# Kernel optimization log

Hardware: AMD Instinct MI355X
Metric: run time of the kernel (lower is better)

The kernel has to match this reference:

```python
import jax, jax.numpy as jnp
import numpy as np

N_NODES = 100000
N_EDGES = 1600000
IN_C = 256
H1 = 128
H2 = 64
OUT_C = 64


def setup_inputs() -> dict:
    key = jax.random.key(0)
    ks = jax.random.split(key, 8)
    x = jax.random.normal(ks[0], (N_NODES, IN_C), dtype=jnp.float32)
    edge_src = jax.random.randint(ks[1], (N_EDGES,), 0, N_NODES, dtype=jnp.int32)
    edge_dst = jax.random.randint(ks[2], (N_EDGES,), 0, N_NODES, dtype=jnp.int32)
    edge_weight = jax.random.uniform(ks[3], (N_EDGES,), dtype=jnp.float32)
    W1 = jax.random.normal(ks[4], (IN_C, H1), dtype=jnp.float32) / np.sqrt(IN_C)
    b1 = jnp.zeros((H1,), dtype=jnp.float32)
    W2 = jax.random.normal(ks[5], (H1, H2), dtype=jnp.float32) / np.sqrt(H1)
    b2 = jnp.zeros((H2,), dtype=jnp.float32)
    W3 = jax.random.normal(ks[6], (H2, OUT_C), dtype=jnp.float32) / np.sqrt(H2)
    b3 = jnp.zeros((OUT_C,), dtype=jnp.float32)
    return dict(x=x, edge_src=edge_src, edge_dst=edge_dst, edge_weight=edge_weight,
                W1=W1, b1=b1, W2=W2, b2=b2, W3=W3, b3=b3)


def _gcn_layer(h, W, b, src, dst, ew):
    # GraphConvolution: out = adj @ (h @ W) + b, adj given as weighted edge list
    support = h @ W                      # [N, d_out] dense GEMM
    msg = support[src] * ew[:, None]     # [E, d_out] gather (irregular access)
    agg = jax.ops.segment_sum(msg, dst, num_segments=N_NODES)  # SpMM scatter-add
    return agg + b


def reference(x, edge_src, edge_dst, edge_weight, W1, b1, W2, b2, W3, b3):
    # Eval-mode forward: dropout is identity (training=False)
    h = jax.nn.relu(_gcn_layer(x, W1, b1, edge_src, edge_dst, edge_weight))
    h = jax.nn.relu(_gcn_layer(h, W2, b2, edge_src, edge_dst, edge_weight))
    out = _gcn_layer(h, W3, b3, edge_src, edge_dst, edge_weight)
    return out
```

## Files before the change

### kernel.cpp

```cpp
#include <hip/hip_runtime.h>
#include <hip/hip_bf16.h>


#define EPB 8192

__device__ __forceinline__ unsigned short f2bf(float f) {
    unsigned int u = __float_as_uint(f);
    unsigned int r = (u + 0x7fffu + ((u >> 16) & 1u)) >> 16;
    return (unsigned short)r;
}

using frag_ab = __attribute__((ext_vector_type(8))) short;
using frag_cd = __attribute__((ext_vector_type(4))) float;

template <int BN, bool ABF16>
__global__ __launch_bounds__(256) void mfma_gemm_kernel(
    const void* __restrict__ Av, const unsigned short* __restrict__ WT,
    unsigned short* __restrict__ C, int M, int K)
{
    constexpr int BM = 128, BK = 64;
    constexpr int LDA = BK + 8;
    __shared__ unsigned short As[BM * LDA];
    __shared__ unsigned short Bs[BN * LDA];

    const int tid = threadIdx.x;
    const int wave = tid >> 6;
    const int lane = tid & 63;
    const int quad = lane >> 4;
    const int l16 = lane & 15;
    const int m0 = blockIdx.x * BM;

    frag_cd acc[2][BN / 16];
#pragma unroll
    for (int rt = 0; rt < 2; ++rt)
#pragma unroll
        for (int f = 0; f < BN / 16; ++f) acc[rt][f] = (frag_cd){0.f, 0.f, 0.f, 0.f};

    for (int k0 = 0; k0 < K; k0 += BK) {
        if constexpr (!ABF16) {
            const float* A = (const float*)Av;
#pragma unroll
            for (int i = 0; i < 8; ++i) {
                const int linear = (i * 256 + tid) * 4;
                const int r = linear >> 6;
                const int c = linear & 63;
                const int row = m0 + r;
                float4 v = make_float4(0.f, 0.f, 0.f, 0.f);
                if (row < M) v = *(const float4*)&A[(size_t)row * K + k0 + c];
                ushort4 u;
                u.x = f2bf(v.x); u.y = f2bf(v.y); u.z = f2bf(v.z); u.w = f2bf(v.w);
                *(ushort4*)&As[r * LDA + c] = u;
            }
        } else {
            const unsigned short* A = (const unsigned short*)Av;
#pragma unroll
            for (int i = 0; i < 4; ++i) {
                const int linear = (i * 256 + tid) * 8;
                const int r = linear >> 6;
                const int c = linear & 63;
                const int row = m0 + r;
                uint4 u = make_uint4(0u, 0u, 0u, 0u);
                if (row < M) u = *(const uint4*)&A[(size_t)row * K + k0 + c];
                *(uint4*)&As[r * LDA + c] = u;
            }
        }
#pragma unroll
        for (int i = 0; i < BN / 32; ++i) {
            const int linear = (i * 256 + tid) * 8;
            const int n = linear >> 6;
            const int c = linear & 63;
            const uint4 u = *(const uint4*)&WT[(size_t)n * K + k0 + c];
            *(uint4*)&Bs[n * LDA + c] = u;
        }
        __syncthreads();

#pragma unroll
        for (int ks = 0; ks < 2; ++ks) {
            const int kk = ks * 32 + quad * 8;
            const frag_ab a0 = *(const frag_ab*)&As[(wave * 32 + l16) * LDA + kk];
            const frag_ab a1 = *(const frag_ab*)&As[(wave * 32 + 16 + l16) * LDA + kk];
#pragma unroll
            for (int f = 0; f < BN / 16; ++f) {
                const frag_ab b = *(const frag_ab*)&Bs[(f * 16 + l16) * LDA + kk];
                acc[0][f] = __builtin_amdgcn_mfma_f32_16x16x32_bf16(a0, b, acc[0][f], 0, 0, 0);
                acc[1][f] = __builtin_amdgcn_mfma_f32_16x16x32_bf16(a1, b, acc[1][f], 0, 0, 0);
            }
        }
        __syncthreads();
    }

#pragma unroll
    for (int rt = 0; rt < 2; ++rt)
#pragma unroll
        for (int f = 0; f < BN / 16; ++f)
#pragma unroll
            for (int r = 0; r < 4; ++r) {
                const int row = m0 + wave * 32 + rt * 16 + quad * 4 + r;
                if (row < M) C[(size_t)row * BN + f * 16 + l16] = f2bf(acc[rt][f][r]);
            }
}

__global__ __launch_bounds__(256) void wt_kernel(
    const float* __restrict__ W1, const float* __restrict__ W2, const float* __restrict__ W3,
    unsigned short* __restrict__ WT1, unsigned short* __restrict__ WT2, unsigned short* __restrict__ WT3)
{
    const int i = blockIdx.x * 256 + threadIdx.x;
    const float* W; unsigned short* WT; int K, N, j;
    if (i < 32768)      { W = W1; WT = WT1; K = 256; N = 128; j = i; }
    else if (i < 40960) { W = W2; WT = WT2; K = 128; N = 64;  j = i - 32768; }
    else if (i < 45056) { W = W3; WT = WT3; K = 64;  N = 64;  j = i - 40960; }
    else return;
    const int n = j / K, k = j % K;
    WT[j] = f2bf(W[k * N + n]);
}

__global__ __launch_bounds__(256) void count_kernel(
    const int* __restrict__ dst, int* __restrict__ cmat, int E, int nblk, int nbuck)
{
    __shared__ int hist[1600];
    for (int i = threadIdx.x; i < nbuck; i += 256) hist[i] = 0;
    __syncthreads();
    const int base = blockIdx.x * EPB;
    const int end = min(base + EPB, E);
    for (int e = base + threadIdx.x; e < end; e += 256)
        atomicAdd(&hist[dst[e] >> 6], 1);
    __syncthreads();
    for (int i = threadIdx.x; i < nbuck; i += 256)
        cmat[(size_t)i * nblk + blockIdx.x] = hist[i];
}

__global__ __launch_bounds__(256) void scanA_kernel(
    int* __restrict__ data, int* __restrict__ psum, int L)
{
    __shared__ int tmp[256];
    const int b0 = blockIdx.x * 1024 + threadIdx.x * 4;
    int v[4] = {0, 0, 0, 0};
    if (b0 + 3 < L) { const int4 t = *(const int4*)&data[b0]; v[0]=t.x; v[1]=t.y; v[2]=t.z; v[3]=t.w; }
    else { for (int i = 0; i < 4; ++i) if (b0 + i < L) v[i] = data[b0 + i]; }
    const int s = v[0] + v[1] + v[2] + v[3];
    tmp[threadIdx.x] = s;
    __syncthreads();
#pragma unroll
    for (int d = 1; d < 256; d <<= 1) {
        const int t = (threadIdx.x >= d) ? tmp[threadIdx.x - d] : 0;
        __syncthreads();
        tmp[threadIdx.x] += t;
        __syncthreads();
    }
    int run = tmp[threadIdx.x] - s;
    int o[4];
#pragma unroll
    for (int i = 0; i < 4; ++i) { o[i] = run; run += v[i]; }
    if (b0 + 3 < L) { *(int4*)&data[b0] = make_int4(o[0], o[1], o[2], o[3]); }
    else { for (int i = 0; i < 4; ++i) if (b0 + i < L) data[b0 + i] = o[i]; }
    if (threadIdx.x == 255) psum[blockIdx.x] = tmp[255];
}

__global__ __launch_bounds__(1024) void scanB_kernel(int* __restrict__ psum, int nb)
{
    __shared__ int tmp[1024];
    const int v = ((int)threadIdx.x < nb) ? psum[threadIdx.x] : 0;
    tmp[threadIdx.x] = v;
    __syncthreads();
#pragma unroll
    for (int d = 1; d < 1024; d <<= 1) {
        const int t = ((int)threadIdx.x >= d) ? tmp[threadIdx.x - d] : 0;
        __syncthreads();
        tmp[threadIdx.x] += t;
        __syncthreads();
    }
    if ((int)threadIdx.x < nb) psum[threadIdx.x] = tmp[threadIdx.x] - v;
}

__global__ __launch_bounds__(256) void scanC_kernel(
    int* __restrict__ data, const int* __restrict__ psum, int L)
{
    const int i = blockIdx.x * 256 + threadIdx.x;
    if (i < L) data[i] += psum[i >> 10];
}

__global__ __launch_bounds__(256) void place_kernel(
    const int* __restrict__ src, const int* __restrict__ dst, const float* __restrict__ ew,
    const int* __restrict__ cmat, uint2* __restrict__ ebuck, int E, int nblk, int nbuck)
{
    __shared__ int cursor[1600];
    const int k = blockIdx.x;
    for (int i = threadIdx.x; i < nbuck; i += 256)
        cursor[i] = cmat[(size_t)i * nblk + k];
    __syncthreads();
    const int base = k * EPB;
    const int end = min(base + EPB, E);
    for (int e = base + threadIdx.x; e < end; e += 256) {
        const int d = dst[e];
        const int b = d >> 6;
        const int pos = atomicAdd(&cursor[b], 1);
        ebuck[pos] = make_uint2(((unsigned)src[e] << 6) | (unsigned)(d & 63),
                                __float_as_uint(ew[e]));
    }
}

__global__ __launch_bounds__(256) void sort2_kernel(
    const uint2* __restrict__ ebuck, const int* __restrict__ cmat,
    int* __restrict__ offs, uint2* __restrict__ ecsr,
    int N, int nblk, int nbuck, int E)
{
    __shared__ int cnt[64];
    __shared__ int cur[64];
    const int b = blockIdx.x;
    const int node0 = b << 6;
    const int nn = min(64, N - node0);
    const int j0 = cmat[(size_t)b * nblk];
    const int j1 = (b + 1 < nbuck) ? cmat[(size_t)(b + 1) * nblk] : E;

    if (threadIdx.x < 64) cnt[threadIdx.x] = 0;
    __syncthreads();
    for (int j = j0 + (int)threadIdx.x; j < j1; j += 256)
        atomicAdd(&cnt[ebuck[j].x & 63u], 1);
    __syncthreads();

    if (threadIdx.x < 64) {
        const int myv = cnt[threadIdx.x];
        int v = myv;
#pragma unroll
        for (int d = 1; d < 64; d <<= 1) {
            const int t = __shfl_up(v, d, 64);
            if ((int)threadIdx.x >= d) v += t;
        }
        const int base = j0 + v - myv;
        cur[threadIdx.x] = base;
        if ((int)threadIdx.x < nn) offs[node0 + threadIdx.x] = base;
        if (threadIdx.x == 0 && b == nbuck - 1) offs[N] = E;
    }
    __syncthreads();

    for (int j = j0 + (int)threadIdx.x; j < j1; j += 256) {
        const uint2 ed = ebuck[j];
        const int pos = atomicAdd(&cur[ed.x & 63u], 1);
        ecsr[pos] = make_uint2(ed.x >> 6, ed.y);
    }
}

template <int D, int LOGT, bool RELU, typename OUT_T>
__global__ __launch_bounds__(256) void gather_agg_kernel(
    const unsigned short* __restrict__ S, const int* __restrict__ offs,
    const uint2* __restrict__ ecsr,
    const float* __restrict__ bias, OUT_T* __restrict__ out, int N)
{
    constexpr int TPN = 1 << LOGT;
    const int gid = blockIdx.x * 256 + threadIdx.x;
    const int node = gid >> LOGT;
    if (node >= N) return;
    const int lane = gid & (TPN - 1);
    const int c8 = lane << 3;

    const int j0 = offs[node];
    const int j1 = offs[node + 1];

    float acc[8];
#pragma unroll
    for (int c = 0; c < 8; ++c) acc[c] = 0.f;

    int jb = j0;
    for (; jb + TPN <= j1; jb += TPN) {
        const uint2 p = ecsr[jb + lane];
        const int myc = (int)p.x;
        const float myw = __uint_as_float(p.y);
#pragma unroll
        for (int t = 0; t < TPN; ++t) {
            const int s = __shfl(myc, t, TPN);
            const float w = __shfl(myw, t, TPN);
            const uint4 v = *(const uint4*)&S[(size_t)s * D + c8];
#pragma unroll
            for (int q = 0; q < 4; ++q) {
                const unsigned int u = (&v.x)[q];
                acc[q * 2 + 0] += w * __uint_as_float(u << 16);
                acc[q * 2 + 1] += w * __uint_as_float(u & 0xffff0000u);
            }
        }
    }
    if (jb < j1) {
        const int j = jb + lane;
        int myc = 0;
        float myw = 0.f;
        if (j < j1) {
            const uint2 p = ecsr[j];
            myc = (int)p.x;
            myw = __uint_as_float(p.y);
        }
        const int cnt = j1 - jb;
        for (int t = 0; t < cnt; ++t) {
            const int s = __shfl(myc, t, TPN);
            const float w = __shfl(myw, t, TPN);
            const uint4 v = *(const uint4*)&S[(size_t)s * D + c8];
#pragma unroll
            for (int q = 0; q < 4; ++q) {
                const unsigned int u = (&v.x)[q];
                acc[q * 2 + 0] += w * __uint_as_float(u << 16);
                acc[q * 2 + 1] += w * __uint_as_float(u & 0xffff0000u);
            }
        }
    }

#pragma unroll
    for (int c = 0; c < 8; ++c) {
        float v = acc[c] + bias[c8 + c];
        if (RELU) v = fmaxf(v, 0.f);
        acc[c] = v;
    }
    if constexpr (sizeof(OUT_T) == 2) {
        uint4 u;
        u.x = ((unsigned)f2bf(acc[1]) << 16) | (unsigned)f2bf(acc[0]);
        u.y = ((unsigned)f2bf(acc[3]) << 16) | (unsigned)f2bf(acc[2]);
        u.z = ((unsigned)f2bf(acc[5]) << 16) | (unsigned)f2bf(acc[4]);
        u.w = ((unsigned)f2bf(acc[7]) << 16) | (unsigned)f2bf(acc[6]);
        *(uint4*)&((unsigned short*)out)[(size_t)node * D + c8] = u;
    } else {
        float* op = (float*)out + (size_t)node * D + c8;
        *(float4*)op = make_float4(acc[0], acc[1], acc[2], acc[3]);
        *((float4*)op + 1) = make_float4(acc[4], acc[5], acc[6], acc[7]);
    }
}

extern "C" void kernel_launch(void* const* d_in, const int* in_sizes, int n_in,
                              void* d_out, int out_size, void* d_ws, size_t ws_size,
                              hipStream_t stream)
{
    const float* x    = (const float*)d_in[0];
    const int*   esrc = (const int*)  d_in[1];
    const int*   edst = (const int*)  d_in[2];
    const float* ew   = (const float*)d_in[3];
    const float* W1   = (const float*)d_in[4];
    const float* b1   = (const float*)d_in[5];
    const float* W2   = (const float*)d_in[6];
    const float* b2   = (const float*)d_in[7];
    const float* W3   = (const float*)d_in[8];
    const float* b3   = (const float*)d_in[9];

    const int N = in_sizes[0] / 256;
    const int E = in_sizes[1];

    const int nbuck = (N + 63) >> 6;
    const int nblk = (E + EPB - 1) / EPB;
    const int L = nbuck * nblk;

    unsigned short* Sb = (unsigned short*)d_ws;
    unsigned short* Hb = Sb + (size_t)N * 128;
    unsigned short* WT1 = Hb + (size_t)N * 128;
    unsigned short* WT2 = WT1 + 256 * 128;
    unsigned short* WT3 = WT2 + 128 * 64;
    uint2* ebuck = (uint2*)(WT3 + 64 * 64);
    uint2* ecsr  = ebuck + E;
    int* offs   = (int*)(ecsr + E);
    int* cmat   = offs + N + 4;
    int* psum   = cmat + ((L + 3) & ~3);
    float* out  = (float*)d_out;

    const dim3 blk(256);
    const int mblocks = (N + 127) / 128;

    wt_kernel<<<(45056 + 255) / 256, blk, 0, stream>>>(W1, W2, W3, WT1, WT2, WT3);
    count_kernel<<<nblk, blk, 0, stream>>>(edst, cmat, E, nblk, nbuck);
    scanA_kernel<<<(L + 1023) / 1024, blk, 0, stream>>>(cmat, psum, L);
    scanB_kernel<<<1, 1024, 0, stream>>>(psum, (L + 1023) / 1024);
    scanC_kernel<<<(L + 255) / 256, blk, 0, stream>>>(cmat, psum, L);
    place_kernel<<<nblk, blk, 0, stream>>>(esrc, edst, ew, cmat, ebuck, E, nblk, nbuck);
    sort2_kernel<<<nbuck, blk, 0, stream>>>(ebuck, cmat, offs, ecsr, N, nblk, nbuck, E);

    mfma_gemm_kernel<128, false><<<mblocks, blk, 0, stream>>>(x, WT1, Sb, N, 256);
    gather_agg_kernel<128, 4, true, unsigned short><<<((N * 16) + 255) / 256, blk, 0, stream>>>(
        Sb, offs, ecsr, b1, Hb, N);

    mfma_gemm_kernel<64, true><<<mblocks, blk, 0, stream>>>(Hb, WT2, Sb, N, 128);
    gather_agg_kernel<64, 3, true, unsigned short><<<((N * 8) + 255) / 256, blk, 0, stream>>>(
        Sb, offs, ecsr, b2, Hb, N);

    mfma_gemm_kernel<64, true><<<mblocks, blk, 0, stream>>>(Hb, WT3, Sb, N, 64);
    gather_agg_kernel<64, 3, false, float><<<((N * 8) + 255) / 256, blk, 0, stream>>>(
        Sb, offs, ecsr, b3, out, N);
}
```

Before: 461.3 us.

## Load GEMM A fragments directly to registers and prefetch next K tile

The MFMA GEMM no longer stages A through shared memory. Each lane loads its own A fragment straight from global memory into registers, converting to bf16 in registers in the fp32 case. The B tile and the next A tile are prefetched into registers while the current tile computes, giving register double-buffering. K becomes a template parameter so the loop is fully unrolled. This removes LDS traffic and the serialized load-then-compute stalls, at the cost of more registers and less coalesced A reads, since each lane fetches 16–32 bytes per row.

```diff
diff --git a/kernel.cpp b/kernel.cpp
--- a/kernel.cpp
+++ b/kernel.cpp
@@ -13,15 +13,16 @@
 using frag_ab = __attribute__((ext_vector_type(8))) short;
 using frag_cd = __attribute__((ext_vector_type(4))) float;
 
-template <int BN, bool ABF16>
+template <int BN, int K, bool ABF16>
 __global__ __launch_bounds__(256) void mfma_gemm_kernel(
     const void* __restrict__ Av, const unsigned short* __restrict__ WT,
-    unsigned short* __restrict__ C, int M, int K)
+    unsigned short* __restrict__ C, int M)
 {
     constexpr int BM = 128, BK = 64;
-    constexpr int LDA = BK + 8;
-    __shared__ unsigned short As[BM * LDA];
-    __shared__ unsigned short Bs[BN * LDA];
+    constexpr int NT = K / BK;
+    constexpr int LDB = BK + 8;
+    constexpr int BLD = BN / 32;
+    __shared__ unsigned short Bs[BN * LDB];
 
     const int tid = threadIdx.x;
     const int wave = tid >> 6;
@@ -30,60 +31,108 @@
     const int l16 = lane & 15;
     const int m0 = blockIdx.x * BM;
 
+    const int r0 = m0 + wave * 32 + l16;
+    const int r1 = r0 + 16;
+    const bool rv[2] = { r0 < M, r1 < M };
+    const int rr[2] = { r0, r1 };
+
     frag_cd acc[2][BN / 16];
 #pragma unroll
     for (int rt = 0; rt < 2; ++rt)
 #pragma unroll
         for (int f = 0; f < BN / 16; ++f) acc[rt][f] = (frag_cd){0.f, 0.f, 0.f, 0.f};
 
-    for (int k0 = 0; k0 < K; k0 += BK) {
-        if constexpr (!ABF16) {
-            const float* A = (const float*)Av;
-#pragma unroll
-            for (int i = 0; i < 8; ++i) {
-                const int linear = (i * 256 + tid) * 4;
-                const int r = linear >> 6;
-                const int c = linear & 63;
-                const int row = m0 + r;
-                float4 v = make_float4(0.f, 0.f, 0.f, 0.f);
-                if (row < M) v = *(const float4*)&A[(size_t)row * K + k0 + c];
-                ushort4 u;
-                u.x = f2bf(v.x); u.y = f2bf(v.y); u.z = f2bf(v.z); u.w = f2bf(v.w);
-                *(ushort4*)&As[r * LDA + c] = u;
-            }
-        } else {
-            const unsigned short* A = (const unsigned short*)Av;
-#pragma unroll
-            for (int i = 0; i < 4; ++i) {
-                const int linear = (i * 256 + tid) * 8;
-                const int r = linear >> 6;
-                const int c = linear & 63;
-                const int row = m0 + r;
-                uint4 u = make_uint4(0u, 0u, 0u, 0u);
-                if (row < M) u = *(const uint4*)&A[(size_t)row * K + k0 + c];
-                *(uint4*)&As[r * LDA + c] = u;
-            }
-        }
-#pragma unroll
-        for (int i = 0; i < BN / 32; ++i) {
+    const float* Af = (const float*)Av;
+    const unsigned short* Ah = (const unsigned short*)Av;
+
+    uint4 breg[BLD];
+    float4 arf[2][2][2];
+    frag_ab arh[2][2];
+
+    auto loadB = [&](int k0) {
+#pragma unroll
+        for (int i = 0; i < BLD; ++i) {
             const int linear = (i * 256 + tid) * 8;
             const int n = linear >> 6;
             const int c = linear & 63;
-            const uint4 u = *(const uint4*)&WT[(size_t)n * K + k0 + c];
-            *(uint4*)&Bs[n * LDA + c] = u;
-        }
-        __syncthreads();
+            breg[i] = *(const uint4*)&WT[(size_t)n * K + k0 + c];
+        }
+    };
+    auto writeB = [&]() {
+#pragma unroll
+        for (int i = 0; i < BLD; ++i) {
+            const int linear = (i * 256 + tid) * 8;
+            const int n = linear >> 6;
+            const int c = linear & 63;
+            *(uint4*)&Bs[n * LDB + c] = breg[i];
+        }
+    };
+    auto loadA = [&](int k0) {
+#pragma unroll
+        for (int rt = 0; rt < 2; ++rt) {
+            if constexpr (!ABF16) {
+                const float* base = &Af[(size_t)rr[rt] * K + k0 + quad * 8];
+#pragma unroll
+                for (int ks = 0; ks < 2; ++ks) {
+                    float4 lo = make_float4(0.f, 0.f, 0.f, 0.f);
+                    float4 hi = make_float4(0.f, 0.f, 0.f, 0.f);
+                    if (rv[rt]) {
+                        lo = *(const float4*)(base + ks * 32);
+                        hi = *(const float4*)(base + ks * 32 + 4);
+                    }
+                    arf[rt][ks][0] = lo;
+                    arf[rt][ks][1] = hi;
+                }
+            } else {
+                const unsigned short* base = &Ah[(size_t)rr[rt] * K + k0 + quad * 8];
+#pragma unroll
+                for (int ks = 0; ks < 2; ++ks) {
+                    frag_ab f = (frag_ab){0, 0, 0, 0, 0, 0, 0, 0};
+                    if (rv[rt]) f = *(const frag_ab*)(base + ks * 32);
+                    arh[rt][ks] = f;
+                }
+            }
+        }
+    };
+
+    loadB(0);
+    loadA(0);
+
+    for (int t = 0; t < NT; ++t) {
+        writeB();
+        __syncthreads();
+
+        frag_ab af[2][2];
+#pragma unroll
+        for (int rt = 0; rt < 2; ++rt)
+#pragma unroll
+            for (int ks = 0; ks < 2; ++ks) {
+                if constexpr (!ABF16) {
+                    const float4 lo = arf[rt][ks][0];
+                    const float4 hi = arf[rt][ks][1];
+                    frag_ab f;
+                    f[0] = (short)f2bf(lo.x); f[1] = (short)f2bf(lo.y);
+                    f[2] = (short)f2bf(lo.z); f[3] = (short)f2bf(lo.w);
+                    f[4] = (short)f2bf(hi.x); f[5] = (short)f2bf(hi.y);
+                    f[6] = (short)f2bf(hi.z); f[7] = (short)f2bf(hi.w);
+                    af[rt][ks] = f;
+                } else {
+                    af[rt][ks] = arh[rt][ks];
+                }
+            }
+        if (t + 1 < NT) {
+            loadB((t + 1) * BK);
+            loadA((t + 1) * BK);
+        }
 
 #pragma unroll
         for (int ks = 0; ks < 2; ++ks) {
             const int kk = ks * 32 + quad * 8;
-            const frag_ab a0 = *(const frag_ab*)&As[(wave * 32 + l16) * LDA + kk];
-            const frag_ab a1 = *(const frag_ab*)&As[(wave * 32 + 16 + l16) * LDA + kk];
 #pragma unroll
             for (int f = 0; f < BN / 16; ++f) {
-                const frag_ab b = *(const frag_ab*)&Bs[(f * 16 + l16) * LDA + kk];
-                acc[0][f] = __builtin_amdgcn_mfma_f32_16x16x32_bf16(a0, b, acc[0][f], 0, 0, 0);
-                acc[1][f] = __builtin_amdgcn_mfma_f32_16x16x32_bf16(a1, b, acc[1][f], 0, 0, 0);
+                const frag_ab b = *(const frag_ab*)&Bs[(f * 16 + l16) * LDB + kk];
+                acc[0][f] = __builtin_amdgcn_mfma_f32_16x16x32_bf16(af[0][ks], b, acc[0][f], 0, 0, 0);
+                acc[1][f] = __builtin_amdgcn_mfma_f32_16x16x32_bf16(af[1][ks], b, acc[1][f], 0, 0, 0);
             }
         }
         __syncthreads();
@@ -366,15 +415,15 @@
     place_kernel<<<nblk, blk, 0, stream>>>(esrc, edst, ew, cmat, ebuck, E, nblk, nbuck);
     sort2_kernel<<<nbuck, blk, 0, stream>>>(ebuck, cmat, offs, ecsr, N, nblk, nbuck, E);
 
-    mfma_gemm_kernel<128, false><<<mblocks, blk, 0, stream>>>(x, WT1, Sb, N, 256);
+    mfma_gemm_kernel<128, 256, false><<<mblocks, blk, 0, stream>>>(x, WT1, Sb, N);
     gather_agg_kernel<128, 4, true, unsigned short><<<((N * 16) + 255) / 256, blk, 0, stream>>>(
         Sb, offs, ecsr, b1, Hb, N);
 
-    mfma_gemm_kernel<64, true><<<mblocks, blk, 0, stream>>>(Hb, WT2, Sb, N, 128);
+    mfma_gemm_kernel<64, 128, true><<<mblocks, blk, 0, stream>>>(Hb, WT2, Sb, N);
     gather_agg_kernel<64, 3, true, unsigned short><<<((N * 8) + 255) / 256, blk, 0, stream>>>(
         Sb, offs, ecsr, b2, Hb, N);
 
-    mfma_gemm_kernel<64, true><<<mblocks, blk, 0, stream>>>(Hb, WT3, Sb, N, 64);
+    mfma_gemm_kernel<64, 64, true><<<mblocks, blk, 0, stream>>>(Hb, WT3, Sb, N);
     gather_agg_kernel<64, 3, false, float><<<((N * 8) + 255) / 256, blk, 0, stream>>>(
         Sb, offs, ecsr, b3, out, N);
 }
```

Result: slower. 474.6 us (+2.9%).
